# Optimization experiments

Measured on AMD Instinct MI355X. Metric: run time of the kernel, lower is better.

## Reference

```python
import jax, jax.numpy as jnp
import numpy as np

P, M, DG, F, H, DH = 2000, 150, 2000, 256, 4, 64
N1, N2 = P + M, P + DG          # adj1 nodes (patient+med), adj2 nodes (patient+diag)
E1, E2, EGP, EGM = 137600, 256000, 64000, 4800
GNN_LAYERS = 2
SA_HID = 128


def setup_inputs() -> dict:
    key = jax.random.key(0)
    ks = jax.random.split(key, 32)
    ri = lambda k, n, hi: jax.random.randint(k, (n,), 0, hi, dtype=jnp.int32)
    rn = lambda k, shape, scale: (jax.random.normal(k, shape, dtype=jnp.float32) * scale)
    inp = {
        'adj1_rows': ri(ks[0], E1, N1), 'adj1_cols': ri(ks[1], E1, N1),
        'adj1_vals': jax.random.uniform(ks[2], (E1,), dtype=jnp.float32),
        'adj2_rows': ri(ks[3], E2, N2), 'adj2_cols': ri(ks[4], E2, N2),
        'adj2_vals': jax.random.uniform(ks[5], (E2,), dtype=jnp.float32),
        'g0_src': ri(ks[6], EGP, P), 'g0_dst': ri(ks[7], EGP, P),
        'g1_src': ri(ks[8], EGP, P), 'g1_dst': ri(ks[9], EGP, P),
        'g2_src': ri(ks[10], EGM, M), 'g2_dst': ri(ks[11], EGM, M),
        'g3_src': ri(ks[12], EGM, M), 'g3_dst': ri(ks[13], EGM, M),
        'keepRate': 1,
        # learned parameters (xavier-ish scales)
        'pEmbed': rn(ks[14], (P, F), 0.05),
        'mEmbed': rn(ks[15], (M, F), 0.05),
        'dEmbed': rn(ks[16], (DG, F), 0.05),
        'gat_W': rn(ks[17], (4, F, H * DH), (2.0 / (F + H * DH)) ** 0.5),
        'gat_al': rn(ks[18], (4, H, DH), 0.1),
        'gat_ar': rn(ks[19], (4, H, DH), 0.1),
        'gat_b': jnp.zeros((4, H * DH), dtype=jnp.float32),
        'sa_W1': rn(ks[20], (H * DH, SA_HID), (2.0 / (H * DH + SA_HID)) ** 0.5),
        'sa_b1': jnp.zeros((SA_HID,), dtype=jnp.float32),
        'sa_W2': rn(ks[21], (SA_HID, 1), 0.1),
        'out_W': rn(ks[22], (2 * F, M), (2.0 / (2 * F + M)) ** 0.5),
        'out_b': jnp.zeros((M,), dtype=jnp.float32),
    }
    return inp


def _spmm(rows, cols, vals, x, n):
    # sparse adj @ x via gather + segment_sum
    return jax.ops.segment_sum(vals[:, None] * x[cols], rows, num_segments=n)


def _seg_softmax(e, seg, n):
    m = jax.ops.segment_max(e, seg, num_segments=n)          # [n, H]
    ex = jnp.exp(e - m[seg])
    s = jax.ops.segment_sum(ex, seg, num_segments=n)
    return ex / (s[seg] + 1e-9)


def _gat(h, W, al, ar, b, src, dst, n):
    # DGL GATConv, feat/attn dropout = 0, negative_slope = 0.2, activation = elu
    feat = (h @ W).reshape(n, H, DH)                          # [n, H, DH]
    el = (feat * al[None]).sum(-1)                            # [n, H]
    er = (feat * ar[None]).sum(-1)
    e = jax.nn.leaky_relu(el[src] + er[dst], negative_slope=0.2)  # [E, H]
    alpha = _seg_softmax(e, dst, n)                           # softmax over in-edges per dst
    out = jax.ops.segment_sum(alpha[:, :, None] * feat[src], dst, num_segments=n)
    out = out + b.reshape(1, H, DH)
    return jax.nn.elu(out).reshape(n, H * DH)


def _sem_att(z, W1, b1, W2):
    # z: [N, K, F]; shared projection; beta over K meta-paths
    w = (jnp.tanh(z @ W1 + b1) @ W2).mean(0)                  # [K, 1]
    beta = jax.nn.softmax(w, axis=0)                          # [K, 1]
    return (beta[None] * z).sum(1)                            # [N, F]


def reference(adj1_rows, adj1_cols, adj1_vals, adj2_rows, adj2_cols, adj2_vals,
              g0_src, g0_dst, g1_src, g1_dst, g2_src, g2_dst, g3_src, g3_dst,
              keepRate, pEmbed, mEmbed, dEmbed, gat_W, gat_al, gat_ar, gat_b,
              sa_W1, sa_b1, sa_W2, out_W, out_b):
    embeds1 = jnp.concatenate([pEmbed, mEmbed], axis=0)       # [N1, F]
    embeds2 = jnp.concatenate([pEmbed, dEmbed], axis=0)       # [N2, F]
    lat1, lat2 = embeds1, embeds2
    acc1 = jnp.zeros_like(embeds1)
    acc2 = jnp.zeros_like(embeds2)
    for _ in range(GNN_LAYERS):
        lat1 = jax.nn.leaky_relu(_spmm(adj1_rows, adj1_cols, adj1_vals, lat1, N1), negative_slope=0.5)
        lat2 = jax.nn.leaky_relu(_spmm(adj2_rows, adj2_cols, adj2_vals, lat2, N2), negative_slope=0.5)
        acc1 = acc1 + lat1
        acc2 = acc2 + lat2
    p1, m_gcn = acc1[:P], acc1[P:]
    p2, d_gcn = acc2[:P], acc2[P:]

    e0 = _gat(p1, gat_W[0], gat_al[0], gat_ar[0], gat_b[0], g0_src, g0_dst, P)
    e1 = _gat(p2, gat_W[1], gat_al[1], gat_ar[1], gat_b[1], g1_src, g1_dst, P)
    e2 = _gat(m_gcn, gat_W[2], gat_al[2], gat_ar[2], gat_b[2], g2_src, g2_dst, M)
    e3 = _gat(m_gcn, gat_W[3], gat_al[3], gat_ar[3], gat_b[3], g3_src, g3_dst, M)

    patient = _sem_att(jnp.stack([e0, e1], axis=1), sa_W1, sa_b1, sa_W2)  # [P, F]
    med = _sem_att(jnp.stack([e2, e3], axis=1), sa_W1, sa_b1, sa_W2)      # [M, F]

    # broadcasted pairwise concat -> ReLU -> Linear -> sum over pairing axis
    pm = jnp.concatenate([
        jnp.broadcast_to(patient[:, None, :], (P, M, F)),
        jnp.broadcast_to(med[None, :, :], (P, M, F)),
    ], axis=-1).reshape(P * M, 2 * F)
    simi = (jax.nn.relu(pm) @ out_W + out_b).reshape(P, M, M)
    simi_pm = simi.sum(axis=1)                                # [P, M]
    return (simi_pm, d_gcn, med, m_gcn, patient)
```

## Files before the change

### kernel.cpp

```cpp
#include <hip/hip_runtime.h>
#include <hip/hip_fp16.h>
#include <cmath>
#include <cstdint>

constexpr int P  = 2000, M = 150, DG = 2000, F = 256, H = 4, DH = 64;
constexpr int N1 = P + M;
constexpr int N2 = P + DG;
constexpr int E1 = 137600, E2 = 256000, EGP = 64000, EGM = 4800;
constexpr int SA_HID = 128;

constexpr int HO1 = E1, HO2 = E1 + E2, HO3 = HO2 + EGP, HO4 = HO3 + EGP,
              HO5 = HO4 + EGM, HOE = HO5 + EGM;

constexpr int CAP_A = 160;
constexpr int CAP_G = 96;
constexpr int OVF_CAP = 4096;

constexpr int CPAD = 16;

__device__ __forceinline__ float4 h4_to_f4(const __half* p) {
  union { ushort4 u4; __half2 h2[2]; } u;
  u.u4 = *(const ushort4*)p;
  float2 lo = __half22float2(u.h2[0]);
  float2 hi = __half22float2(u.h2[1]);
  return make_float4(lo.x, lo.y, hi.x, hi.y);
}
__device__ __forceinline__ void f4_to_h4(__half* p, float4 v) {
  union { ushort4 u4; __half2 h2[2]; } u;
  u.h2[0] = __float22half2_rn(make_float2(v.x, v.y));
  u.h2[1] = __float22half2_rn(make_float2(v.z, v.w));
  *(ushort4*)p = u.u4;
}

constexpr int CAST_CH = (P * F + M * F + DG * F) / 8;

__global__ __launch_bounds__(256) void k_build(
    const int* __restrict__ a1r, const int* __restrict__ a1c, const float* __restrict__ a1v,
    const int* __restrict__ a2r, const int* __restrict__ a2c, const float* __restrict__ a2v,
    const int* __restrict__ d0, const int* __restrict__ s0,
    const int* __restrict__ d1, const int* __restrict__ s1,
    const int* __restrict__ d2, const int* __restrict__ s2,
    const int* __restrict__ d3, const int* __restrict__ s3,
    int* cur1, uint2* ell1, int* cur2, uint2* ell2,
    int* cu0, unsigned* eg0, int* cu1, unsigned* eg1,
    int* cu2, unsigned* eg2, int* cu3, unsigned* eg3,
    int* __restrict__ ovf_n, int4* __restrict__ ovf,
    const float* __restrict__ pEf, const float* __restrict__ mEf,
    const float* __restrict__ dEf,
    __half* __restrict__ pEh, __half* __restrict__ mEh, __half* __restrict__ dEh) {
  int tid = blockIdx.x * 256 + threadIdx.x;
  int T = gridDim.x * 256;
  int seg[4], row[4]; unsigned p0[4], p1[4];
#pragma unroll
  for (int u = 0; u < 4; ++u) {
    int i = tid + u * T;
    seg[u] = -1;
    if (i < HOE) {
      if (i < HO1)      { seg[u] = 0; row[u] = a1r[i]; p0[u] = (unsigned)a1c[i]; p1[u] = __float_as_uint(a1v[i]); }
      else if (i < HO2) { int j = i - HO1; seg[u] = 1; row[u] = a2r[j]; p0[u] = (unsigned)a2c[j]; p1[u] = __float_as_uint(a2v[j]); }
      else if (i < HO3) { int j = i - HO2; seg[u] = 2; row[u] = d0[j]; p0[u] = (unsigned)s0[j]; }
      else if (i < HO4) { int j = i - HO3; seg[u] = 3; row[u] = d1[j]; p0[u] = (unsigned)s1[j]; }
      else if (i < HO5) { int j = i - HO4; seg[u] = 4; row[u] = d2[j]; p0[u] = (unsigned)s2[j]; }
      else              { int j = i - HO5; seg[u] = 5; row[u] = d3[j]; p0[u] = (unsigned)s3[j]; }
    }
  }
#pragma unroll
  for (int u = 0; u < 4; ++u) {
    int r = row[u];
    switch (seg[u]) {
      case 0: { int slot = atomicAdd(&cur1[(size_t)r * CPAD], 1);
        if (slot < CAP_A) ell1[(size_t)r * CAP_A + slot] = make_uint2(p0[u], p1[u]);
        else { int o = atomicAdd(&ovf_n[0], 1); if (o < OVF_CAP) ovf[0 * OVF_CAP + o] = make_int4(r, (int)p0[u], (int)p1[u], 0); } } break;
      case 1: { int slot = atomicAdd(&cur2[(size_t)r * CPAD], 1);
        if (slot < CAP_A) ell2[(size_t)r * CAP_A + slot] = make_uint2(p0[u], p1[u]);
        else { int o = atomicAdd(&ovf_n[1], 1); if (o < OVF_CAP) ovf[1 * OVF_CAP + o] = make_int4(r, (int)p0[u], (int)p1[u], 0); } } break;
      case 2: { int slot = atomicAdd(&cu0[(size_t)r * CPAD], 1);
        if (slot < CAP_G) eg0[(size_t)r * CAP_G + slot] = p0[u];
        else { int o = atomicAdd(&ovf_n[2], 1); if (o < OVF_CAP) ovf[2 * OVF_CAP + o] = make_int4(r, (int)p0[u], 0, 0); } } break;
      case 3: { int slot = atomicAdd(&cu1[(size_t)r * CPAD], 1);
        if (slot < CAP_G) eg1[(size_t)r * CAP_G + slot] = p0[u];
        else { int o = atomicAdd(&ovf_n[3], 1); if (o < OVF_CAP) ovf[3 * OVF_CAP + o] = make_int4(r, (int)p0[u], 0, 0); } } break;
      case 4: { int slot = atomicAdd(&cu2[(size_t)r * CPAD], 1);
        if (slot < CAP_G) eg2[(size_t)r * CAP_G + slot] = p0[u];
        else { int o = atomicAdd(&ovf_n[4], 1); if (o < OVF_CAP) ovf[4 * OVF_CAP + o] = make_int4(r, (int)p0[u], 0, 0); } } break;
      case 5: { int slot = atomicAdd(&cu3[(size_t)r * CPAD], 1);
        if (slot < CAP_G) eg3[(size_t)r * CAP_G + slot] = p0[u];
        else { int o = atomicAdd(&ovf_n[5], 1); if (o < OVF_CAP) ovf[5 * OVF_CAP + o] = make_int4(r, (int)p0[u], 0, 0); } } break;
      default: break;
    }
  }
  for (int c = tid; c < CAST_CH; c += T) {
    int j = c * 8;
    const float* src; __half* dst;
    if (j < P * F)              { src = pEf + j;               dst = pEh + j; }
    else if (j < P * F + M * F) { src = mEf + (j - P * F);     dst = mEh + (j - P * F); }
    else                        { src = dEf + (j - P*F - M*F); dst = dEh + (j - P*F - M*F); }
    float4 a = *(const float4*)src, b = *(const float4*)(src + 4);
    f4_to_h4(dst, a);
    f4_to_h4(dst + 4, b);
  }
}

template<int LAYER>
__global__ __launch_bounds__(256) void k_spmm(
    const int* __restrict__ cur1, const uint2* __restrict__ ell1,
    const int* __restrict__ cur2, const uint2* __restrict__ ell2,
    const int* __restrict__ ovf_n, const int4* __restrict__ ovf,
    const __half* __restrict__ pEh, const __half* __restrict__ mEh,
    const __half* __restrict__ dEh,
    float* __restrict__ lat1f, float* __restrict__ lat2f,
    __half* __restrict__ lat1h, __half* __restrict__ lat2h,
    float* __restrict__ acc1, float* __restrict__ acc2,
    float* __restrict__ out_mgcn, float* __restrict__ out_dgcn) {
  int gw = (blockIdx.x * 256 + threadIdx.x) >> 6;
  if (gw >= N1 + N2) return;
  int lane = threadIdx.x & 63;
  bool g2 = gw >= N1;
  int row = g2 ? gw - N1 : gw;
  const uint2* pe = (g2 ? ell2 : ell1) + (size_t)row * CAP_A;
  const __half* latinh = g2 ? lat2h : lat1h;
  const __half* tailEh = g2 ? dEh : mEh;
  int deg = (g2 ? cur2 : cur1)[(size_t)row * CPAD];
  int dn = deg < CAP_A ? deg : CAP_A;
  int fo = lane << 2;
  float4 s = {0.f, 0.f, 0.f, 0.f};
  auto fetch = [&](int c) -> float4 {
    const __half* b;
    if (LAYER == 1) b = (c < P) ? (pEh + (size_t)c * F) : (tailEh + (size_t)(c - P) * F);
    else            b = latinh + (size_t)c * F;
    return h4_to_f4(b + fo);
  };
  int i = 0;
  for (; i + 8 <= dn; i += 8) {
    uint2 m[8]; float4 a[8];
#pragma unroll
    for (int u = 0; u < 8; ++u) m[u] = pe[i + u];
#pragma unroll
    for (int u = 0; u < 8; ++u) a[u] = fetch((int)m[u].x);
#pragma unroll
    for (int u = 0; u < 8; ++u) {
      float v = __uint_as_float(m[u].y);
      s.x += v * a[u].x; s.y += v * a[u].y; s.z += v * a[u].z; s.w += v * a[u].w;
    }
  }
  for (; i + 4 <= dn; i += 4) {
    uint2 m0 = pe[i], m1 = pe[i + 1], m2 = pe[i + 2], m3 = pe[i + 3];
    float v0 = __uint_as_float(m0.y), v1 = __uint_as_float(m1.y),
          v2 = __uint_as_float(m2.y), v3 = __uint_as_float(m3.y);
    float4 a0 = fetch((int)m0.x), a1 = fetch((int)m1.x),
           a2 = fetch((int)m2.x), a3 = fetch((int)m3.x);
    s.x += v0 * a0.x + v1 * a1.x + v2 * a2.x + v3 * a3.x;
    s.y += v0 * a0.y + v1 * a1.y + v2 * a2.y + v3 * a3.y;
    s.z += v0 * a0.z + v1 * a1.z + v2 * a2.z + v3 * a3.z;
    s.w += v0 * a0.w + v1 * a1.w + v2 * a2.w + v3 * a3.w;
  }
  for (; i < dn; ++i) {
    uint2 m = pe[i];
    float v = __uint_as_float(m.y);
    float4 a = fetch((int)m.x);
    s.x += v * a.x; s.y += v * a.y; s.z += v * a.z; s.w += v * a.w;
  }
  {
    int gi = g2 ? 1 : 0;
    int on = ovf_n[gi];
    if (on > 0) {
      const int4* ol = ovf + gi * OVF_CAP;
      for (int k = 0; k < on; ++k) {
        int4 e = ol[k];
        if (e.x == row) {
          float v = __int_as_float(e.z);
          float4 a = fetch(e.y);
          s.x += v * a.x; s.y += v * a.y; s.z += v * a.z; s.w += v * a.w;
        }
      }
    }
  }
  float4 l;
  l.x = s.x > 0.f ? s.x : 0.5f * s.x;
  l.y = s.y > 0.f ? s.y : 0.5f * s.y;
  l.z = s.z > 0.f ? s.z : 0.5f * s.z;
  l.w = s.w > 0.f ? s.w : 0.5f * s.w;
  if (LAYER == 1) {
    *(float4*)((g2 ? lat2f : lat1f) + (size_t)row * F + fo) = l;
    f4_to_h4((g2 ? lat2h : lat1h) + (size_t)row * F + fo, l);
  } else {
    const float* latf = g2 ? lat2f : lat1f;
    float4 b = *(const float4*)(latf + (size_t)row * F + fo);
    float4 a = {b.x + l.x, b.y + l.y, b.z + l.z, b.w + l.w};
    *(float4*)((g2 ? acc2 : acc1) + (size_t)row * F + fo) = a;
    if (row >= P)
      *(float4*)((g2 ? out_dgcn : out_mgcn) + (size_t)(row - P) * F + fo) = a;
  }
}

constexpr int FR  = 16;
constexpr int NB0 = (P + FR - 1) / FR;
constexpr int NB2 = (M + FR - 1) / FR;
constexpr int FEAT_BLOCKS = 2 * NB0 + 2 * NB2;

__global__ __launch_bounds__(256) void k_gat_feat_all(
    const float* __restrict__ acc1, const float* __restrict__ acc2,
    const float* __restrict__ gat_W, const float* __restrict__ gat_al,
    const float* __restrict__ gat_ar,
    __half* __restrict__ f0, __half* __restrict__ f1,
    __half* __restrict__ f2, __half* __restrict__ f3,
    float* __restrict__ el, float* __restrict__ er) {
  int b = blockIdx.x;
  int g, rb, n; const float* h; __half* fout;
  if (b < NB0)            { g = 0; rb = b;              n = P; h = acc1; fout = f0; }
  else if (b < 2 * NB0)   { g = 1; rb = b - NB0;        n = P; h = acc2; fout = f1; }
  else if (b < 2*NB0+NB2) { g = 2; rb = b - 2 * NB0;    n = M; h = acc1 + (size_t)P * F; fout = f2; }
  else                    { g = 3; rb = b - 2*NB0 - NB2; n = M; h = acc1 + (size_t)P * F; fout = f3; }
  int elo = (g == 0) ? 0 : (g == 1) ? P * H : (g == 2) ? 2 * P * H : (2 * P + M) * H;
  const float* W = gat_W + (size_t)g * F * F;
  __shared__ float hs[FR][F];
  int t = threadIdx.x;
  int r0 = rb * FR;
  for (int q = t; q < FR * 64; q += 256) {
    int r = q >> 6, ln = q & 63;
    int row = r0 + r;
    float4 v = {0.f, 0.f, 0.f, 0.f};
    if (row < n) v = *(const float4*)(h + (size_t)row * F + (ln << 2));
    *(float4*)&hs[r][ln << 2] = v;
  }
  __syncthreads();
  float acc[FR];
#pragma unroll
  for (int r = 0; r < FR; ++r) acc[r] = 0.f;
  for (int k = 0; k < F; k += 4) {
    float w0 = W[(size_t)k * F + t],       w1 = W[(size_t)(k + 1) * F + t],
          w2 = W[(size_t)(k + 2) * F + t], w3 = W[(size_t)(k + 3) * F + t];
#pragma unroll
    for (int r = 0; r < FR; ++r) {
      float4 h4 = *(const float4*)&hs[r][k];
      acc[r] += h4.x * w0 + h4.y * w1 + h4.z * w2 + h4.w * w3;
    }
  }
  int head = t >> 6, d = t & 63;
  float av = gat_al[g * H * DH + head * DH + d];
  float rv = gat_ar[g * H * DH + head * DH + d];
#pragma unroll
  for (int r = 0; r < FR; ++r) {
    int row = r0 + r;
    if (row < n) {
      fout[(size_t)row * F + t] = __float2half_rn(acc[r]);
      float cl = acc[r] * av, cr = acc[r] * rv;
      for (int o = 32; o > 0; o >>= 1) {
        cl += __shfl_down(cl, o, 64);
        cr += __shfl_down(cr, o, 64);
      }
      if (d == 0) { el[elo + row * H + head] = cl; er[elo + row * H + head] = cr; }
    }
  }
}

__global__ __launch_bounds__(256) void k_gat_agg_all(
    const int* __restrict__ cu0, const unsigned* __restrict__ eg0,
    const int* __restrict__ cu1, const unsigned* __restrict__ eg1,
    const int* __restrict__ cu2, const unsigned* __restrict__ eg2,
    const int* __restrict__ cu3, const unsigned* __restrict__ eg3,
    const int* __restrict__ ovf_n, const int4* __restrict__ ovf,
    const float* __restrict__ el, const float* __restrict__ er,
    const __half* __restrict__ f0, const __half* __restrict__ f1,
    const __half* __restrict__ f2, const __half* __restrict__ f3,
    const float* __restrict__ gat_b,
    float* __restrict__ e0, float* __restrict__ e1,
    float* __restrict__ e2, float* __restrict__ e3) {
  int gw = (blockIdx.x * 256 + threadIdx.x) >> 6;
  if (gw >= 2 * P + 2 * M) return;
  int lane = threadIdx.x & 63;
  int g, row; const int* cu; const unsigned* eg; const __half* feat; float* out; int elo;
  if (gw < P)            { g = 0; row = gw;             cu = cu0; eg = eg0; feat = f0; out = e0; elo = 0; }
  else if (gw < 2 * P)   { g = 1; row = gw - P;         cu = cu1; eg = eg1; feat = f1; out = e1; elo = P * H; }
  else if (gw < 2*P + M) { g = 2; row = gw - 2 * P;     cu = cu2; eg = eg2; feat = f2; out = e2; elo = 2 * P * H; }
  else                   { g = 3; row = gw - 2 * P - M; cu = cu3; eg = eg3; feat = f3; out = e3; elo = (2 * P + M) * H; }
  int head = lane >> 4;
  int fo = lane << 2;
  const float* elb = el + elo;
  float erv = er[elo + row * H + head];
  int deg = cu[(size_t)row * CPAD];
  int dn = deg < CAP_G ? deg : CAP_G;
  const unsigned* ps = eg + (size_t)row * CAP_G;
  int on = ovf_n[2 + g];
  const int4* ol = ovf + (2 + g) * OVF_CAP;
  float mx = -3.4e38f;
  int i = 0;
  for (; i + 4 <= dn; i += 4) {
    int s0 = (int)ps[i], s1 = (int)ps[i + 1], s2 = (int)ps[i + 2], s3 = (int)ps[i + 3];
    float a = elb[s0 * H + head] + erv, b = elb[s1 * H + head] + erv,
          c = elb[s2 * H + head] + erv, d = elb[s3 * H + head] + erv;
    a = a > 0.f ? a : 0.2f * a; b = b > 0.f ? b : 0.2f * b;
    c = c > 0.f ? c : 0.2f * c; d = d > 0.f ? d : 0.2f * d;
    mx = fmaxf(mx, fmaxf(fmaxf(a, b), fmaxf(c, d)));
  }
  for (; i < dn; ++i) {
    float a = elb[(int)ps[i] * H + head] + erv;
    a = a > 0.f ? a : 0.2f * a;
    mx = fmaxf(mx, a);
  }
  if (on > 0) {
    for (int k = 0; k < on; ++k) {
      int4 e = ol[k];
      if (e.x == row) {
        float a = elb[e.y * H + head] + erv;
        a = a > 0.f ? a : 0.2f * a;
        mx = fmaxf(mx, a);
      }
    }
  }
  float ssum = 0.f;
  float4 acc = {0.f, 0.f, 0.f, 0.f};
  i = 0;
  for (; i + 2 <= dn; i += 2) {
    int s0 = (int)ps[i], s1 = (int)ps[i + 1];
    float a = elb[s0 * H + head] + erv; a = a > 0.f ? a : 0.2f * a;
    float b = elb[s1 * H + head] + erv; b = b > 0.f ? b : 0.2f * b;
    float x0 = expf(a - mx), x1 = expf(b - mx);
    float4 q0 = h4_to_f4(feat + (size_t)s0 * F + fo);
    float4 q1 = h4_to_f4(feat + (size_t)s1 * F + fo);
    ssum += x0 + x1;
    acc.x += x0 * q0.x + x1 * q1.x;
    acc.y += x0 * q0.y + x1 * q1.y;
    acc.z += x0 * q0.z + x1 * q1.z;
    acc.w += x0 * q0.w + x1 * q1.w;
  }
  for (; i < dn; ++i) {
    int s0 = (int)ps[i];
    float a = elb[s0 * H + head] + erv; a = a > 0.f ? a : 0.2f * a;
    float x0 = expf(a - mx);
    float4 q0 = h4_to_f4(feat + (size_t)s0 * F + fo);
    ssum += x0;
    acc.x += x0 * q0.x; acc.y += x0 * q0.y; acc.z += x0 * q0.z; acc.w += x0 * q0.w;
  }
  if (on > 0) {
    for (int k = 0; k < on; ++k) {
      int4 e = ol[k];
      if (e.x == row) {
        float a = elb[e.y * H + head] + erv; a = a > 0.f ? a : 0.2f * a;
        float x0 = expf(a - mx);
        float4 q0 = h4_to_f4(feat + (size_t)e.y * F + fo);
        ssum += x0;
        acc.x += x0 * q0.x; acc.y += x0 * q0.y; acc.z += x0 * q0.z; acc.w += x0 * q0.w;
      }
    }
  }
  float inv = 1.f / (ssum + 1e-9f);
  const float* bb = gat_b + g * F + fo;
  float4 v = {acc.x * inv + bb[0], acc.y * inv + bb[1],
              acc.z * inv + bb[2], acc.w * inv + bb[3]};
  v.x = v.x > 0.f ? v.x : expm1f(v.x);
  v.y = v.y > 0.f ? v.y : expm1f(v.y);
  v.z = v.z > 0.f ? v.z : expm1f(v.z);
  v.w = v.w > 0.f ? v.w : expm1f(v.w);
  *(float4*)(out + (size_t)row * F + fo) = v;
}

constexpr int SR  = 16;
constexpr int SB0 = (P + SR - 1) / SR;
constexpr int SB2 = (M + SR - 1) / SR;
constexpr int SEM_BLOCKS = 2 * SB0 + 2 * SB2;

__global__ __launch_bounds__(128) void k_sem_w_all(
    const float* __restrict__ e0, const float* __restrict__ e1,
    const float* __restrict__ e2, const float* __restrict__ e3,
    const float* __restrict__ W1, const float* __restrict__ b1,
    const float* __restrict__ W2, float* __restrict__ w) {
  int b = blockIdx.x;
  int zid, rb, n; const float* z;
  if (b < SB0)            { zid = 0; rb = b;             n = P; z = e0; }
  else if (b < 2 * SB0)   { zid = 1; rb = b - SB0;       n = P; z = e1; }
  else if (b < 2*SB0+SB2) { zid = 2; rb = b - 2 * SB0;   n = M; z = e2; }
  else                    { zid = 3; rb = b - 2*SB0-SB2; n = M; z = e3; }
  __shared__ float zs[SR][F];
  int t = threadIdx.x;
  int r0 = rb * SR;
  for (int q = t; q < SR * 64; q += 128) {
    int r = q >> 6, ln = q & 63;
    int row = r0 + r;
    float4 v = {0.f, 0.f, 0.f, 0.f};
    if (row < n) v = *(const float4*)(z + (size_t)row * F + (ln << 2));
    *(float4*)&zs[r][ln << 2] = v;
  }
  __syncthreads();
  float hid[SR];
#pragma unroll
  for (int r = 0; r < SR; ++r) hid[r] = b1[t];
  for (int k = 0; k < F; k += 4) {
    float w0 = W1[(size_t)k * SA_HID + t],       w1 = W1[(size_t)(k + 1) * SA_HID + t],
          w2 = W1[(size_t)(k + 2) * SA_HID + t], w3 = W1[(size_t)(k + 3) * SA_HID + t];
#pragma unroll
    for (int r = 0; r < SR; ++r) {
      float4 z4 = *(const float4*)&zs[r][k];
      hid[r] += z4.x * w0 + z4.y * w1 + z4.z * w2 + z4.w * w3;
    }
  }
  float w2v = W2[t];
  float local = 0.f;
  for (int r = 0; r < SR; ++r) {
    int row = r0 + r;
    if (row < n) local += tanhf(hid[r]) * w2v;
  }
  for (int o = 32; o > 0; o >>= 1) local += __shfl_down(local, o, 64);
  __shared__ float pp[2];
  if ((t & 63) == 0) pp[t >> 6] = local;
  __syncthreads();
  if (t == 0) atomicAdd(&w[zid], pp[0] + pp[1]);
}

__global__ __launch_bounds__(256) void k_med_cvec(
    const float* __restrict__ e2, const float* __restrict__ e3,
    const float* __restrict__ w, const float* __restrict__ outW,
    const float* __restrict__ outb,
    float* __restrict__ out_med, float* __restrict__ cbuf) {
  int t = threadIdx.x;
  float m0 = w[2] * (1.f / M), m1 = w[3] * (1.f / M);
  float mxv = fmaxf(m0, m1);
  float a0 = expf(m0 - mxv), a1 = expf(m1 - mxv);
  float sc = 1.f / (a0 + a1);
  a0 *= sc; a1 *= sc;
  float4 rs = {0.f, 0.f, 0.f, 0.f};
  for (int j = t; j < M * F / 4; j += 256) {
    float4 u0 = ((const float4*)e2)[j], u1 = ((const float4*)e3)[j];
    float4 r = {a0 * u0.x + a1 * u1.x, a0 * u0.y + a1 * u1.y,
                a0 * u0.z + a1 * u1.z, a0 * u0.w + a1 * u1.w};
    ((float4*)out_med)[j] = r;
    rs.x += r.x > 0.f ? r.x : 0.f;
    rs.y += r.y > 0.f ? r.y : 0.f;
    rs.z += r.z > 0.f ? r.z : 0.f;
    rs.w += r.w > 0.f ? r.w : 0.f;
  }
  __shared__ float4 sv4[4][64];
  sv4[t >> 6][t & 63] = rs;
  __syncthreads();
  __shared__ float sv[F];
  if (t < 64) {
    float4 a = sv4[0][t], b = sv4[1][t], c = sv4[2][t], d = sv4[3][t];
    sv[t * 4 + 0] = a.x + b.x + c.x + d.x;
    sv[t * 4 + 1] = a.y + b.y + c.y + d.y;
    sv[t * 4 + 2] = a.z + b.z + c.z + d.z;
    sv[t * 4 + 3] = a.w + b.w + c.w + d.w;
  }
  __syncthreads();
  if (t < M) {
    float cc = (float)M * outb[t];
    for (int f = 0; f < F; f += 4) {
      cc += sv[f]     * outW[(size_t)(F + f) * M + t]
          + sv[f + 1] * outW[(size_t)(F + f + 1) * M + t]
          + sv[f + 2] * outW[(size_t)(F + f + 2) * M + t]
          + sv[f + 3] * outW[(size_t)(F + f + 3) * M + t];
    }
    cbuf[t] = cc;
  }
}

constexpr int FIN_R = 8;
__global__ __launch_bounds__(256) void k_final(
    const float* __restrict__ e0, const float* __restrict__ e1,
    const float* __restrict__ w, const float* __restrict__ outW,
    const float* __restrict__ c,
    float* __restrict__ out_pat, float* __restrict__ simi) {
  float m0 = w[0] * (1.f / P), m1 = w[1] * (1.f / P);
  float mxv = fmaxf(m0, m1);
  float a0 = expf(m0 - mxv), a1 = expf(m1 - mxv);
  float sc = 1.f / (a0 + a1);
  a0 *= sc; a1 *= sc;
  __shared__ float psh[FIN_R][F];
  int t = threadIdx.x;
  int r0 = blockIdx.x * FIN_R;
  for (int q = t; q < FIN_R * 64; q += 256) {
    int r = q >> 6, ln = q & 63;
    size_t off = (size_t)(r0 + r) * F + (ln << 2);
    float4 u0 = *(const float4*)(e0 + off), u1 = *(const float4*)(e1 + off);
    float4 v = {a0 * u0.x + a1 * u1.x, a0 * u0.y + a1 * u1.y,
                a0 * u0.z + a1 * u1.z, a0 * u0.w + a1 * u1.w};
    *(float4*)(out_pat + off) = v;
    v.x = v.x > 0.f ? v.x : 0.f; v.y = v.y > 0.f ? v.y : 0.f;
    v.z = v.z > 0.f ? v.z : 0.f; v.w = v.w > 0.f ? v.w : 0.f;
    *(float4*)&psh[r][ln << 2] = v;
  }
  __syncthreads();
  if (t < M) {
    float acc[FIN_R];
#pragma unroll
    for (int r = 0; r < FIN_R; ++r) acc[r] = 0.f;
    for (int f = 0; f < F; f += 4) {
      float w0 = outW[(size_t)f * M + t],       w1 = outW[(size_t)(f + 1) * M + t],
            w2 = outW[(size_t)(f + 2) * M + t], w3 = outW[(size_t)(f + 3) * M + t];
#pragma unroll
      for (int r = 0; r < FIN_R; ++r) {
        float4 p4 = *(const float4*)&psh[r][f];
        acc[r] += p4.x * w0 + p4.y * w1 + p4.z * w2 + p4.w * w3;
      }
    }
    float cv = c[t];
    for (int r = 0; r < FIN_R; ++r)
      simi[(size_t)(r0 + r) * M + t] = (float)M * acc[r] + cv;
  }
}

extern "C" void kernel_launch(void* const* d_in, const int* in_sizes, int n_in,
                              void* d_out, int out_size, void* d_ws, size_t ws_size,
                              hipStream_t stream) {
  const int*   adj1_rows = (const int*)d_in[0];
  const int*   adj1_cols = (const int*)d_in[1];
  const float* adj1_vals = (const float*)d_in[2];
  const int*   adj2_rows = (const int*)d_in[3];
  const int*   adj2_cols = (const int*)d_in[4];
  const float* adj2_vals = (const float*)d_in[5];
  const int*   g0_src = (const int*)d_in[6];
  const int*   g0_dst = (const int*)d_in[7];
  const int*   g1_src = (const int*)d_in[8];
  const int*   g1_dst = (const int*)d_in[9];
  const int*   g2_src = (const int*)d_in[10];
  const int*   g2_dst = (const int*)d_in[11];
  const int*   g3_src = (const int*)d_in[12];
  const int*   g3_dst = (const int*)d_in[13];
  const float* pE     = (const float*)d_in[15];
  const float* mE     = (const float*)d_in[16];
  const float* dE     = (const float*)d_in[17];
  const float* gat_W  = (const float*)d_in[18];
  const float* gat_al = (const float*)d_in[19];
  const float* gat_ar = (const float*)d_in[20];
  const float* gat_b  = (const float*)d_in[21];
  const float* sa_W1  = (const float*)d_in[22];
  const float* sa_b1  = (const float*)d_in[23];
  const float* sa_W2  = (const float*)d_in[24];
  const float* out_W  = (const float*)d_in[25];
  const float* out_b  = (const float*)d_in[26];

  int* ip = (int*)d_ws;
  int* cur1 = ip; ip += (size_t)N1 * CPAD;
  int* cur2 = ip; ip += (size_t)N2 * CPAD;
  int* cu0  = ip; ip += (size_t)P * CPAD;
  int* cu1  = ip; ip += (size_t)P * CPAD;
  int* cu2  = ip; ip += (size_t)M * CPAD;
  int* cu3  = ip; ip += (size_t)M * CPAD;
  int* ovf_n = ip; ip += 6;
  float* wbuf = (float*)ip; ip += 4;
  size_t memset_bytes = (size_t)((char*)ip - (char*)d_ws);

  uintptr_t up = ((uintptr_t)ip + 15) & ~(uintptr_t)15;
  int4* ovf = (int4*)up;
  uint2* ell1 = (uint2*)(ovf + 6 * OVF_CAP);
  uint2* ell2 = ell1 + (size_t)N1 * CAP_A;
  unsigned* eg0 = (unsigned*)(ell2 + (size_t)N2 * CAP_A);
  unsigned* eg1 = eg0 + (size_t)P * CAP_G;
  unsigned* eg2 = eg1 + (size_t)P * CAP_G;
  unsigned* eg3 = eg2 + (size_t)M * CAP_G;
  __half* hp = (__half*)(eg3 + (size_t)M * CAP_G);
  __half* pEh   = hp; hp += (size_t)P * F;
  __half* mEh   = hp; hp += (size_t)M * F;
  __half* dEh   = hp; hp += (size_t)DG * F;
  __half* lat1h = hp; hp += (size_t)N1 * F;
  __half* lat2h = hp; hp += (size_t)N2 * F;
  __half* f0h   = hp; hp += (size_t)P * F;
  __half* f1h   = hp; hp += (size_t)P * F;
  __half* f2h   = hp; hp += (size_t)M * F;
  __half* f3h   = hp; hp += (size_t)M * F;
  float* fp = (float*)hp;
  float* lat1f = fp; fp += (size_t)N1 * F;
  float* lat2f = fp; fp += (size_t)N2 * F;
  float* acc1  = fp; fp += (size_t)N1 * F;
  float* acc2  = fp; fp += (size_t)N2 * F;
  float* el    = fp; fp += (size_t)(2 * P + 2 * M) * H;
  float* er    = fp; fp += (size_t)(2 * P + 2 * M) * H;
  float* e0b   = fp; fp += (size_t)P * F;
  float* e1b   = fp; fp += (size_t)P * F;
  float* e2b   = fp; fp += (size_t)M * F;
  float* e3b   = fp; fp += (size_t)M * F;
  float* cbuf  = fp; fp += 256;

  float* out_simi = (float*)d_out;
  float* out_dgcn = out_simi + (size_t)P * M;
  float* out_med  = out_dgcn + (size_t)DG * F;
  float* out_mgcn = out_med  + (size_t)M * F;
  float* out_pat  = out_mgcn + (size_t)M * F;

  hipMemsetAsync(d_ws, 0, memset_bytes, stream);

  int eb = ((HOE + 3) / 4 + 255) / 256;
  k_build<<<eb, 256, 0, stream>>>(adj1_rows, adj1_cols, adj1_vals,
                                  adj2_rows, adj2_cols, adj2_vals,
                                  g0_dst, g0_src, g1_dst, g1_src,
                                  g2_dst, g2_src, g3_dst, g3_src,
                                  cur1, ell1, cur2, ell2,
                                  cu0, eg0, cu1, eg1, cu2, eg2, cu3, eg3,
                                  ovf_n, ovf,
                                  pE, mE, dE, pEh, mEh, dEh);

  int sb = ((N1 + N2) * 64 + 255) / 256;
  k_spmm<1><<<sb, 256, 0, stream>>>(cur1, ell1, cur2, ell2, ovf_n, ovf,
                                    pEh, mEh, dEh, lat1f, lat2f, lat1h, lat2h,
                                    acc1, acc2, out_mgcn, out_dgcn);
  k_spmm<2><<<sb, 256, 0, stream>>>(cur1, ell1, cur2, ell2, ovf_n, ovf,
                                    pEh, mEh, dEh, lat1f, lat2f, lat1h, lat2h,
                                    acc1, acc2, out_mgcn, out_dgcn);

  k_gat_feat_all<<<FEAT_BLOCKS, 256, 0, stream>>>(acc1, acc2, gat_W, gat_al, gat_ar,
                                                  f0h, f1h, f2h, f3h, el, er);
  int ab = ((2 * P + 2 * M) * 64 + 255) / 256;
  k_gat_agg_all<<<ab, 256, 0, stream>>>(cu0, eg0, cu1, eg1, cu2, eg2, cu3, eg3,
                                        ovf_n, ovf, el, er, f0h, f1h, f2h, f3h, gat_b,
                                        e0b, e1b, e2b, e3b);

  k_sem_w_all<<<SEM_BLOCKS, 128, 0, stream>>>(e0b, e1b, e2b, e3b, sa_W1, sa_b1, sa_W2, wbuf);

  k_med_cvec<<<1, 256, 0, stream>>>(e2b, e3b, wbuf, out_W, out_b, out_med, cbuf);

  k_final<<<P / FIN_R, 256, 0, stream>>>(e0b, e1b, wbuf, out_W, cbuf, out_pat, out_simi);
}
```

Baseline: 319.6 us.

## Split each SpMM row across two wavefronts and shrink per-block row tiles

The SpMM kernel now assigns two 64-lane wavefronts to each sparse row. They take alternating nonzeros, and the partial sums are combined through shared memory. The goal is more memory-level parallelism for the gather-bound rows, since the grid now has twice as many waves. Row tile sizes for the GAT feature, semantic-attention and final kernels are also reduced, giving more blocks and better occupancy on the large GPU. This costs a block-wide sync and a shared-memory reduction, and N1+N2 must be even so that no group straddles an out-of-range row; it is even (6150).

```diff
diff --git a/kernel.cpp b/kernel.cpp
--- a/kernel.cpp
+++ b/kernel.cpp
@@ -112,11 +112,12 @@
     __half* __restrict__ lat1h, __half* __restrict__ lat2h,
     float* __restrict__ acc1, float* __restrict__ acc2,
     float* __restrict__ out_mgcn, float* __restrict__ out_dgcn) {
-  int gw = (blockIdx.x * 256 + threadIdx.x) >> 6;
-  if (gw >= N1 + N2) return;
+  int grp = (blockIdx.x * 256 + threadIdx.x) >> 7;
   int lane = threadIdx.x & 63;
-  bool g2 = gw >= N1;
-  int row = g2 ? gw - N1 : gw;
+  int wh   = (threadIdx.x >> 6) & 1;
+  int gl   = threadIdx.x >> 7;
+  bool g2 = grp >= N1;
+  int row = g2 ? grp - N1 : grp;
   const uint2* pe = (g2 ? ell2 : ell1) + (size_t)row * CAP_A;
   const __half* latinh = g2 ? lat2h : lat1h;
   const __half* tailEh = g2 ? dEh : mEh;
@@ -130,11 +131,11 @@
     else            b = latinh + (size_t)c * F;
     return h4_to_f4(b + fo);
   };
-  int i = 0;
-  for (; i + 8 <= dn; i += 8) {
+  int i = wh;
+  for (; i + 15 <= dn; i += 16) {
     uint2 m[8]; float4 a[8];
 #pragma unroll
-    for (int u = 0; u < 8; ++u) m[u] = pe[i + u];
+    for (int u = 0; u < 8; ++u) m[u] = pe[i + 2 * u];
 #pragma unroll
     for (int u = 0; u < 8; ++u) a[u] = fetch((int)m[u].x);
 #pragma unroll
@@ -143,22 +144,19 @@
       s.x += v * a[u].x; s.y += v * a[u].y; s.z += v * a[u].z; s.w += v * a[u].w;
     }
   }
-  for (; i + 4 <= dn; i += 4) {
-    uint2 m0 = pe[i], m1 = pe[i + 1], m2 = pe[i + 2], m3 = pe[i + 3];
-    float v0 = __uint_as_float(m0.y), v1 = __uint_as_float(m1.y),
-          v2 = __uint_as_float(m2.y), v3 = __uint_as_float(m3.y);
-    float4 a0 = fetch((int)m0.x), a1 = fetch((int)m1.x),
-           a2 = fetch((int)m2.x), a3 = fetch((int)m3.x);
-    s.x += v0 * a0.x + v1 * a1.x + v2 * a2.x + v3 * a3.x;
-    s.y += v0 * a0.y + v1 * a1.y + v2 * a2.y + v3 * a3.y;
-    s.z += v0 * a0.z + v1 * a1.z + v2 * a2.z + v3 * a3.z;
-    s.w += v0 * a0.w + v1 * a1.w + v2 * a2.w + v3 * a3.w;
-  }
-  for (; i < dn; ++i) {
+  for (; i < dn; i += 2) {
     uint2 m = pe[i];
     float v = __uint_as_float(m.y);
     float4 a = fetch((int)m.x);
     s.x += v * a.x; s.y += v * a.y; s.z += v * a.z; s.w += v * a.w;
+  }
+  __shared__ float part[2][F];
+  if (wh == 1) *(float4*)&part[gl][fo] = s;
+  __syncthreads();
+  if (wh == 1) return;
+  {
+    float4 p = *(const float4*)&part[gl][fo];
+    s.x += p.x; s.y += p.y; s.z += p.z; s.w += p.w;
   }
   {
     int gi = g2 ? 1 : 0;
@@ -193,7 +191,7 @@
   }
 }
 
-constexpr int FR  = 16;
+constexpr int FR  = 8;
 constexpr int NB0 = (P + FR - 1) / FR;
 constexpr int NB2 = (M + FR - 1) / FR;
 constexpr int FEAT_BLOCKS = 2 * NB0 + 2 * NB2;
@@ -355,7 +353,7 @@
   *(float4*)(out + (size_t)row * F + fo) = v;
 }
 
-constexpr int SR  = 16;
+constexpr int SR  = 4;
 constexpr int SB0 = (P + SR - 1) / SR;
 constexpr int SB2 = (M + SR - 1) / SR;
 constexpr int SEM_BLOCKS = 2 * SB0 + 2 * SB2;
@@ -453,7 +451,7 @@
   }
 }
 
-constexpr int FIN_R = 8;
+constexpr int FIN_R = 4;
 __global__ __launch_bounds__(256) void k_final(
     const float* __restrict__ e0, const float* __restrict__ e1,
     const float* __restrict__ w, const float* __restrict__ outW,
@@ -588,7 +586,7 @@
                                   ovf_n, ovf,
                                   pE, mE, dE, pEh, mEh, dEh);
 
-  int sb = ((N1 + N2) * 64 + 255) / 256;
+  int sb = (N1 + N2) / 2;
   k_spmm<1><<<sb, 256, 0, stream>>>(cur1, ell1, cur2, ell2, ovf_n, ovf,
                                     pEh, mEh, dEh, lat1f, lat2f, lat1h, lat2h,
                                     acc1, acc2, out_mgcn, out_dgcn);
```

Result: no change. 313.9 us (-1.8%).
